# Optimization experiments

Hardware: AMD Instinct MI355X
Metric: run time of the kernel (lower is better)

## Reference

```python
import jax, jax.numpy as jnp
import numpy as np

N_QUBITS = 16
N_LAYERS = 2
NUM_CLASSES = 10
BATCH = 256

# CNOT as (c_out, t_out, c_in, t_in)
_CNOT = np.zeros((2, 2, 2, 2), dtype=np.complex64)
_CNOT[0, 0, 0, 0] = 1; _CNOT[0, 1, 0, 1] = 1
_CNOT[1, 1, 1, 0] = 1; _CNOT[1, 0, 1, 1] = 1
CNOT = jnp.asarray(_CNOT)


def rot_matrix(phi, theta, omega):
    # PennyLane Rot = RZ(omega) @ RY(theta) @ RZ(phi)
    c, s = jnp.cos(theta / 2), jnp.sin(theta / 2)
    m00 = jnp.exp(-0.5j * (phi + omega)) * c
    m01 = -jnp.exp(0.5j * (phi - omega)) * s
    m10 = jnp.exp(-0.5j * (phi - omega)) * s
    m11 = jnp.exp(0.5j * (phi + omega)) * c
    return jnp.stack([jnp.stack([m00, m01]), jnp.stack([m10, m11])]).astype(jnp.complex64)


def apply_1q(state, U, w, n):
    # state: (B, 2**n); wire 0 = most-significant bit (PennyLane convention)
    B = state.shape[0]
    st = state.reshape(B, 2 ** w, 2, -1)
    st = jnp.einsum('oi,baic->baoc', U, st)
    return st.reshape(B, -1)


def apply_cnot(state, c, t, n):
    B = state.shape[0]
    st = state.reshape((B,) + (2,) * n)
    st = jnp.tensordot(CNOT, st, axes=[[2, 3], [c + 1, t + 1]])  # new c,t axes at front
    st = jnp.moveaxis(st, [0, 1], [c + 1, t + 1])
    return st.reshape(B, -1)


def circuit_expvals(x, q_params, n, n_layers):
    # AmplitudeEmbedding with normalize=True
    norm = jnp.sqrt(jnp.sum(x * x, axis=-1, keepdims=True))
    psi = (x / norm).astype(jnp.complex64)
    for l in range(n_layers):
        for w in range(n):
            U = rot_matrix(q_params[l, w, 0], q_params[l, w, 1], q_params[l, w, 2])
            psi = apply_1q(psi, U, w, n)
        r = (l % (n - 1)) + 1  # default StronglyEntanglingLayers ranges
        for w in range(n):
            psi = apply_cnot(psi, w, (w + r) % n, n)
    probs = psi.real ** 2 + psi.imag ** 2  # (B, 2**n)
    B = probs.shape[0]
    ev = []
    for w in range(n):
        p = probs.reshape(B, 2 ** w, 2, -1)
        ev.append(p[:, :, 0, :].sum(axis=(1, 2)) - p[:, :, 1, :].sum(axis=(1, 2)))
    return jnp.stack(ev, axis=1)  # (B, n)


def setup_inputs() -> dict:
    key = jax.random.key(0)
    k1, k2, k3, k4 = jax.random.split(key, 4)
    x = jax.random.normal(k1, (BATCH, 2 ** N_QUBITS), dtype=jnp.float32)
    q_params = jax.random.normal(k2, (N_LAYERS, N_QUBITS, 3), dtype=jnp.float32)
    lim = 1.0 / np.sqrt(N_QUBITS)
    W = jax.random.uniform(k3, (NUM_CLASSES, N_QUBITS), jnp.float32, -lim, lim)
    b = jax.random.uniform(k4, (NUM_CLASSES,), jnp.float32, -lim, lim)
    return {"x": x, "q_params": q_params, "W": W, "b": b}


def reference(x, q_params, W, b):
    feats = circuit_expvals(x, q_params, N_QUBITS, N_LAYERS)  # (B, n_qubits)
    return feats @ W.T + b
```

## Files before the change

kernel.cpp:

```cpp
#include <hip/hip_runtime.h>


#define BATCH 256
#define NCLS 10

typedef float v2f __attribute__((ext_vector_type(2)));
typedef _Float16 f16x2 __attribute__((ext_vector_type(2)));

struct CircuitMeta { unsigned l1mask[16]; unsigned l1role[16]; unsigned fin[16]; };

__host__ __device__ constexpr CircuitMeta make_meta() {
  CircuitMeta m{};
  unsigned col[16], inv[16];
  for (int w = 0; w < 16; ++w) { col[w] = 1u << (15 - w); inv[w] = 1u << (15 - w); }
  for (int w = 0; w < 16; ++w) { int c = w, t = (w + 1) & 15; col[c] ^= col[t]; inv[t] ^= inv[c]; }
  for (int w = 0; w < 16; ++w) { m.l1mask[w] = col[w]; m.l1role[w] = inv[w]; }
  for (int w = 0; w < 16; ++w) { int c = w, t = (w + 2) & 15; col[c] ^= col[t]; inv[t] ^= inv[c]; }
  for (int w = 0; w < 16; ++w) m.fin[w] = inv[w];
  return m;
}
constexpr CircuitMeta META = make_meta();

__host__ __device__ constexpr unsigned HASH(unsigned i) {
  return i ^ ((i >> 4) & 15u) ^ ((i >> 8) & 15u);
}

__device__ __forceinline__ v2f swp(v2f a) { return __builtin_shufflevector(a, a, 1, 0); }

__device__ __forceinline__ unsigned PK(v2f a) {
  return __builtin_bit_cast(unsigned, __builtin_amdgcn_cvt_pkrtz(a.x, a.y));
}
__device__ __forceinline__ v2f UNPK(unsigned u) {
  f16x2 h = __builtin_bit_cast(f16x2, u);
  return (v2f){(float)h.x, (float)h.y};
}

template<int B0,int B1,int B2,int B3,int B4>
__host__ __device__ constexpr unsigned regval5(int j) {
  return ((unsigned)(j & 1) << B0) | ((unsigned)((j >> 1) & 1) << B1) |
         ((unsigned)((j >> 2) & 1) << B2) | ((unsigned)((j >> 3) & 1) << B3) |
         ((unsigned)((j >> 4) & 1) << B4);
}

template<int B0,int B1,int B2,int B3,int B4, unsigned MG, unsigned RG>
__device__ __forceinline__ void gate5(v2f (&A)[32], const float* __restrict__ g,
                                      int gi, unsigned tp) {
  constexpr unsigned cover = (1u<<B0)|(1u<<B1)|(1u<<B2)|(1u<<B3)|(1u<<B4);
  static_assert((MG & ~cover) == 0u, "gate mask not covered by stage reg bits");
  constexpr unsigned mr = ((MG>>B0)&1u) | (((MG>>B1)&1u)<<1) | (((MG>>B2)&1u)<<2)
                        | (((MG>>B3)&1u)<<3) | (((MG>>B4)&1u)<<4);
  static_assert(mr != 0u, "empty reg mask");
  constexpr unsigned pivot = mr & (0u - mr);

  float u00r = g[gi*8+0], u00i = g[gi*8+1], u01r = g[gi*8+2], u01i = g[gi*8+3];
  float u10r = g[gi*8+4], u10i = g[gi*8+5], u11r = g[gi*8+6], u11i = g[gi*8+7];
  const bool s = (__popc(RG & tp) & 1) != 0;
  float e00r = s ? u11r : u00r, e00i = s ? u11i : u00i;
  float e01r = s ? u10r : u01r, e01i = s ? u10i : u01i;
  float e10r = s ? u01r : u10r, e10i = s ? u01i : u10i;
  float e11r = s ? u00r : u11r, e11i = s ? u00i : u11i;
  v2f a00 = {e00r, e00r}, b00 = {-e00i, e00i};
  v2f a01 = {e01r, e01r}, b01 = {-e01i, e01i};
  v2f a10 = {e10r, e10r}, b10 = {-e10i, e10i};
  v2f a11 = {e11r, e11r}, b11 = {-e11i, e11i};

  #pragma unroll
  for (int j0 = 0; j0 < 32; ++j0) {
    if (j0 & (int)pivot) continue;
    const int j1 = j0 ^ (int)mr;
    const bool podd =
      (__builtin_popcount(RG & regval5<B0,B1,B2,B3,B4>(j0)) & 1) != 0;
    v2f v0 = A[j0], v1 = A[j1];
    v2f v0s = swp(v0), v1s = swp(v1);
    if (!podd) {
      A[j0] = a00*v0 + b00*v0s + a01*v1 + b01*v1s;
      A[j1] = a10*v0 + b10*v0s + a11*v1 + b11*v1s;
    } else {
      A[j0] = a11*v0 + b11*v0s + a10*v1 + b10*v1s;
      A[j1] = a01*v0 + b01*v0s + a00*v1 + b00*v1s;
    }
  }
}

__global__ void prep_gates(const float* __restrict__ qp, float* __restrict__ g) {
  int i = threadIdx.x;
  if (i >= 32) return;
  float phi = qp[i*3+0], th = qp[i*3+1], om = qp[i*3+2];
  float cth = cosf(0.5f*th), sth = sinf(0.5f*th);
  float a = 0.5f*(phi+om), d = 0.5f*(phi-om);
  float ca = cosf(a), sa = sinf(a), cd = cosf(d), sd = sinf(d);
  g[i*8+0] =  ca*cth; g[i*8+1] = -sa*cth;
  g[i*8+2] = -cd*sth; g[i*8+3] = -sd*sth;
  g[i*8+4] =  cd*sth; g[i*8+5] = -sd*sth;
  g[i*8+6] =  ca*cth; g[i*8+7] =  sa*cth;
}

__global__ __launch_bounds__(256, 4) void passA(const float* __restrict__ x,
    unsigned* __restrict__ st, const float* __restrict__ g) {
  __shared__ unsigned L[8192];
  const int t = threadIdx.x;
  const int batch = blockIdx.x >> 3;
  const unsigned f = blockIdx.x & 7;
  const float* xb = x + ((size_t)batch << 16) + ((size_t)f << 13);

  v2f A[32];
  #pragma unroll
  for (int j = 0; j < 32; ++j) A[j] = (v2f){xb[((unsigned)j << 8) | (unsigned)t], 0.f};

  gate5<8,9,10,11,12, 0x1000u,0x1000u>(A, g, 3, 0u);
  gate5<8,9,10,11,12, 0x0800u,0x0800u>(A, g, 4, 0u);
  gate5<8,9,10,11,12, 0x0400u,0x0400u>(A, g, 5, 0u);
  gate5<8,9,10,11,12, 0x0200u,0x0200u>(A, g, 6, 0u);
  gate5<8,9,10,11,12, 0x0100u,0x0100u>(A, g, 7, 0u);

  {
    const unsigned wb = HASH((unsigned)t);
    #pragma unroll
    for (int j = 0; j < 32; ++j) L[wb ^ HASH((unsigned)j << 8)] = PK(A[j]);
    __syncthreads();
    const unsigned rb = HASH((((unsigned)t & 0xF8u) << 5) | ((unsigned)t & 7u));
    #pragma unroll
    for (int j = 0; j < 32; ++j) A[j] = UNPK(L[rb ^ HASH((unsigned)j << 3)]);
  }

  gate5<3,4,5,6,7, 0x0080u,0x0080u>(A, g,  8, 0u);
  gate5<3,4,5,6,7, 0x0040u,0x0040u>(A, g,  9, 0u);
  gate5<3,4,5,6,7, 0x0020u,0x0020u>(A, g, 10, 0u);
  gate5<3,4,5,6,7, 0x0010u,0x0010u>(A, g, 11, 0u);
  gate5<3,4,5,6,7, 0x0008u,0x0008u>(A, g, 12, 0u);

  __syncthreads();
  {
    const unsigned wb = HASH((((unsigned)t & 0xF8u) << 5) | ((unsigned)t & 7u));
    #pragma unroll
    for (int j = 0; j < 32; ++j) L[wb ^ HASH((unsigned)j << 3)] = PK(A[j]);
    __syncthreads();
    const unsigned rb = HASH((unsigned)t << 3);
    #pragma unroll
    for (int j = 0; j < 32; ++j)
      A[j] = UNPK(L[rb ^ HASH(((unsigned)j & 7u) | (((unsigned)j & 24u) << 8))]);
  }

  gate5<0,1,2,11,12, 0x0004u,0x0004u>(A, g, 13, 0u);
  gate5<0,1,2,11,12, 0x0002u,0x0002u>(A, g, 14, 0u);
  gate5<0,1,2,11,12, 0x0001u,0x0001u>(A, g, 15, 0u);

  unsigned* outb = st + ((size_t)batch << 16) + ((size_t)f << 13);
  #pragma unroll
  for (int jh = 0; jh < 4; ++jh) {
    uint4 q0, q1;
    q0.x = PK(A[jh*8+0]); q0.y = PK(A[jh*8+1]); q0.z = PK(A[jh*8+2]); q0.w = PK(A[jh*8+3]);
    q1.x = PK(A[jh*8+4]); q1.y = PK(A[jh*8+5]); q1.z = PK(A[jh*8+6]); q1.w = PK(A[jh*8+7]);
    const unsigned si = ((unsigned)jh << 11) | ((unsigned)t << 3);
    *(uint4*)(outb + si) = q0;
    *(uint4*)(outb + si + 4) = q1;
  }
}

__global__ __launch_bounds__(256, 4) void passB(unsigned* __restrict__ st,
    const float* __restrict__ g) {
  __shared__ unsigned L[8192];
  const int t = threadIdx.x;
  const int batch = blockIdx.x >> 3;
  const unsigned c = blockIdx.x & 7;
  unsigned* stb = st + ((size_t)batch << 16);

  const unsigned lbase = ((unsigned)t & 127u) | (((unsigned)t & 128u) << 3) | (c << 7);
  v2f A[32];
  #pragma unroll
  for (int j = 0; j < 32; ++j) A[j] = UNPK(stb[((unsigned)j << 11) | lbase]);

  const unsigned tp1 = lbase;
  gate5<11,12,13,14,15, 0x8000u,0x8000u>(A, g, 0, tp1);
  gate5<11,12,13,14,15, 0x4000u,0x4000u>(A, g, 1, tp1);
  gate5<11,12,13,14,15, 0x2000u,0x2000u>(A, g, 2, tp1);
  gate5<11,12,13,14,15, META.l1mask[0], META.l1role[0]>(A, g, 16, tp1);
  gate5<11,12,13,14,15, META.l1mask[1], META.l1role[1]>(A, g, 17, tp1);
  gate5<11,12,13,14,15, META.l1mask[2], META.l1role[2]>(A, g, 18, tp1);
  gate5<11,12,13,14,15, META.l1mask[3], META.l1role[3]>(A, g, 19, tp1);

  {
    const unsigned wb = HASH((unsigned)t);
    #pragma unroll
    for (int j = 0; j < 32; ++j) L[wb ^ HASH((unsigned)j << 8)] = PK(A[j]);
    __syncthreads();
    const unsigned rb = HASH((((unsigned)t & 0xF0u) << 5) | (((unsigned)t & 15u) << 1));
    #pragma unroll
    for (int j = 0; j < 32; ++j)
      A[j] = UNPK(L[rb ^ HASH(((unsigned)j & 1u) | (((unsigned)j & 30u) << 4))]);
  }

  const unsigned tp2 = (((unsigned)t & 0xF0u) << 8) | (((unsigned)t & 15u) << 1) | (c << 7);
  gate5<0,5,6,10,11, META.l1mask[4], META.l1role[4]>(A, g, 20, tp2);
  gate5<0,5,6,10,11, META.l1mask[9], META.l1role[9]>(A, g, 25, tp2);

  __syncthreads();
  {
    const unsigned wb = HASH((((unsigned)t & 0xF0u) << 5) | (((unsigned)t & 15u) << 1));
    #pragma unroll
    for (int j = 0; j < 32; ++j)
      L[wb ^ HASH(((unsigned)j & 1u) | (((unsigned)j & 30u) << 4))] = PK(A[j]);
    __syncthreads();
    const unsigned rb = HASH((((unsigned)t & 0xFEu) << 5) | ((unsigned)t & 1u));
    #pragma unroll
    for (int j = 0; j < 32; ++j) A[j] = UNPK(L[rb ^ HASH((unsigned)j << 1)]);
  }

  const unsigned tp3 = (((unsigned)t & 0xFCu) << 8) | (((unsigned)t & 2u) << 5)
                     | ((unsigned)t & 1u) | (c << 7);
  gate5<1,2,3,4,5, META.l1mask[10], META.l1role[10]>(A, g, 26, tp3);
  gate5<1,2,3,4,5, META.l1mask[11], META.l1role[11]>(A, g, 27, tp3);
  gate5<1,2,3,4,5, META.l1mask[12], META.l1role[12]>(A, g, 28, tp3);
  gate5<1,2,3,4,5, META.l1mask[13], META.l1role[13]>(A, g, 29, tp3);

  __syncthreads();
  {
    const unsigned wb = HASH((((unsigned)t & 0xFEu) << 5) | ((unsigned)t & 1u));
    #pragma unroll
    for (int j = 0; j < 32; ++j) L[wb ^ HASH((unsigned)j << 1)] = PK(A[j]);
    __syncthreads();
    const unsigned rb = HASH((unsigned)t << 2);
    #pragma unroll
    for (int j = 0; j < 32; ++j)
      A[j] = UNPK(L[rb ^ HASH(((unsigned)j & 3u) | (((unsigned)j & 28u) << 8))]);
  }

  const unsigned tp4 = (((unsigned)t & 0xE0u) << 5) | (((unsigned)t & 31u) << 2) | (c << 7);
  gate5<0,1,13,14,15, META.l1mask[14], META.l1role[14]>(A, g, 30, tp4);
  gate5<0,1,13,14,15, META.l1mask[15], META.l1role[15]>(A, g, 31, tp4);

  #pragma unroll
  for (int jh = 0; jh < 8; ++jh) {
    uint4 q;
    q.x = PK(A[jh*4+0]); q.y = PK(A[jh*4+1]); q.z = PK(A[jh*4+2]); q.w = PK(A[jh*4+3]);
    *(uint4*)(stb + (tp4 | ((unsigned)jh << 13))) = q;
  }
}

__global__ __launch_bounds__(256, 4) void passC(const unsigned* __restrict__ st,
    const float* __restrict__ g, float* __restrict__ partials) {
  __shared__ float R[4][17];
  const int t = threadIdx.x;
  const int batch = blockIdx.x >> 3;
  const unsigned f = blockIdx.x & 7;
  const unsigned* stb = st + ((size_t)batch << 16);

  const unsigned cbase = (f << 13) | (((unsigned)t & 192u) << 5) | ((unsigned)t & 63u);
  v2f A[32];
  #pragma unroll
  for (int j = 0; j < 32; ++j) A[j] = UNPK(stb[cbase | ((unsigned)j << 6)]);

  gate5<6,7,8,9,10, META.l1mask[5], META.l1role[5]>(A, g, 21, cbase);
  gate5<6,7,8,9,10, META.l1mask[6], META.l1role[6]>(A, g, 22, cbase);
  gate5<6,7,8,9,10, META.l1mask[7], META.l1role[7]>(A, g, 23, cbase);
  gate5<6,7,8,9,10, META.l1mask[8], META.l1role[8]>(A, g, 24, cbase);

  float sv[16], tot = 0.f;
  #pragma unroll
  for (int w = 0; w < 16; ++w) sv[w] = 0.f;
  #pragma unroll
  for (int j = 0; j < 32; ++j) {
    const float pr = A[j].x*A[j].x + A[j].y*A[j].y;
    tot += pr;
    #pragma unroll
    for (int w = 0; w < 16; ++w) {
      const bool neg = (__builtin_popcount(META.fin[w] & ((unsigned)j << 6)) & 1) != 0;
      sv[w] += neg ? -pr : pr;
    }
  }
  #pragma unroll
  for (int w = 0; w < 16; ++w)
    if (__popc(META.fin[w] & cbase) & 1) sv[w] = -sv[w];

  #pragma unroll
  for (int off = 32; off; off >>= 1) {
    tot += __shfl_xor(tot, off, 64);
    #pragma unroll
    for (int w = 0; w < 16; ++w) sv[w] += __shfl_xor(sv[w], off, 64);
  }
  const int wave = t >> 6, lane = t & 63;
  if (lane == 0) {
    #pragma unroll
    for (int w = 0; w < 16; ++w) R[wave][w] = sv[w];
    R[wave][16] = tot;
  }
  __syncthreads();
  if (t < 17) {
    const float s2 = R[0][t] + R[1][t] + R[2][t] + R[3][t];
    partials[(size_t)blockIdx.x * 17 + t] = s2;
  }
}

__global__ __launch_bounds__(64) void head(const float* __restrict__ partials,
    const float* __restrict__ W, const float* __restrict__ bias,
    float* __restrict__ out) {
  const int b = blockIdx.x, tid = threadIdx.x;
  __shared__ float red[17];
  __shared__ float ev[16];
  if (tid < 17) {
    float s = 0.f;
    #pragma unroll
    for (int ch = 0; ch < 8; ++ch) s += partials[(size_t)((b << 3) + ch) * 17 + tid];
    red[tid] = s;
  }
  __syncthreads();
  if (tid < 16) ev[tid] = red[tid] / red[16];
  __syncthreads();
  if (tid < NCLS) {
    float o = bias[tid];
    #pragma unroll
    for (int w = 0; w < 16; ++w) o += ev[w] * W[tid*16 + w];
    out[b*NCLS + tid] = o;
  }
}

extern "C" void kernel_launch(void* const* d_in, const int* in_sizes, int n_in,
                              void* d_out, int out_size, void* d_ws, size_t ws_size,
                              hipStream_t stream) {
  const float* x  = (const float*)d_in[0];
  const float* qp = (const float*)d_in[1];
  const float* W  = (const float*)d_in[2];
  const float* bv = (const float*)d_in[3];
  float* out = (float*)d_out;

  unsigned* st     = (unsigned*)d_ws;
  float*    gates  = (float*)((char*)d_ws + (size_t)BATCH * 65536 * 4);
  float*    parts  = (float*)((char*)gates + 1024);

  prep_gates<<<dim3(1), dim3(64), 0, stream>>>(qp, gates);
  passA<<<dim3(BATCH*8), dim3(256), 0, stream>>>(x, st, gates);
  passB<<<dim3(BATCH*8), dim3(256), 0, stream>>>(st, gates);
  passC<<<dim3(BATCH*8), dim3(256), 0, stream>>>(st, gates, parts);
  head<<<dim3(BATCH), dim3(64), 0, stream>>>(parts, W, bv, out);
}
```

Before: 207.8 us.

## Switch state registers to split real/imag planes for packed FMA gates

The per-thread state moves from 32 interleaved complex values to 16 real and 16 imaginary two-wide vectors, where the two lanes hold a pair of amplitudes differing in one qubit bit. The gate kernel is rewritten for this layout, with separate paths for register-pair, lane-only and mixed gates, so the complex arithmetic maps onto packed FMA without swaps for most gates. All loads, LDS transposes and stores are rewritten to pack and unpack the new layout, and the final reduction is vectorised too. The goal is fewer VALU instructions per gate; the cost is more complex coefficient setup and possible register pressure.

```diff
diff --git a/kernel.cpp b/kernel.cpp
--- a/kernel.cpp
+++ b/kernel.cpp
@@ -6,6 +6,8 @@
 
 typedef float v2f __attribute__((ext_vector_type(2)));
 typedef _Float16 f16x2 __attribute__((ext_vector_type(2)));
+
+#define KATTR __launch_bounds__(256, 4)
 
 struct CircuitMeta { unsigned l1mask[16]; unsigned l1role[16]; unsigned fin[16]; };
 
@@ -25,61 +27,126 @@
   return i ^ ((i >> 4) & 15u) ^ ((i >> 8) & 15u);
 }
 
+__device__ __forceinline__ unsigned PKS(float r, float i) {
+  return __builtin_bit_cast(unsigned, __builtin_amdgcn_cvt_pkrtz(r, i));
+}
+__device__ __forceinline__ v2f vfma(v2f a, v2f b, v2f c) {
+  return __builtin_elementwise_fma(a, b, c);
+}
 __device__ __forceinline__ v2f swp(v2f a) { return __builtin_shufflevector(a, a, 1, 0); }
 
-__device__ __forceinline__ unsigned PK(v2f a) {
-  return __builtin_bit_cast(unsigned, __builtin_amdgcn_cvt_pkrtz(a.x, a.y));
-}
-__device__ __forceinline__ v2f UNPK(unsigned u) {
-  f16x2 h = __builtin_bit_cast(f16x2, u);
-  return (v2f){(float)h.x, (float)h.y};
-}
-
-template<int B0,int B1,int B2,int B3,int B4>
-__host__ __device__ constexpr unsigned regval5(int j) {
-  return ((unsigned)(j & 1) << B0) | ((unsigned)((j >> 1) & 1) << B1) |
-         ((unsigned)((j >> 2) & 1) << B2) | ((unsigned)((j >> 3) & 1) << B3) |
-         ((unsigned)((j >> 4) & 1) << B4);
-}
-
-template<int B0,int B1,int B2,int B3,int B4, unsigned MG, unsigned RG>
-__device__ __forceinline__ void gate5(v2f (&A)[32], const float* __restrict__ g,
+__device__ __forceinline__ float esel(int q, int pos, float e00, float e01,
+                                      float e10, float e11) {
+  int p = q ? 3 - pos : pos;
+  return p == 0 ? e00 : p == 1 ? e01 : p == 2 ? e10 : e11;
+}
+
+template<int KB0,int KB1,int KB2,int KB3,int LB, unsigned MG, unsigned RG>
+__device__ __forceinline__ void gateV(v2f (&Vr)[16], v2f (&Vi)[16],
+                                      const float* __restrict__ g,
                                       int gi, unsigned tp) {
-  constexpr unsigned cover = (1u<<B0)|(1u<<B1)|(1u<<B2)|(1u<<B3)|(1u<<B4);
+  constexpr unsigned cover = (1u<<KB0)|(1u<<KB1)|(1u<<KB2)|(1u<<KB3)|(1u<<LB);
   static_assert((MG & ~cover) == 0u, "gate mask not covered by stage reg bits");
-  constexpr unsigned mr = ((MG>>B0)&1u) | (((MG>>B1)&1u)<<1) | (((MG>>B2)&1u)<<2)
-                        | (((MG>>B3)&1u)<<3) | (((MG>>B4)&1u)<<4);
-  static_assert(mr != 0u, "empty reg mask");
-  constexpr unsigned pivot = mr & (0u - mr);
+  constexpr unsigned mk = ((MG>>KB0)&1u) | (((MG>>KB1)&1u)<<1)
+                        | (((MG>>KB2)&1u)<<2) | (((MG>>KB3)&1u)<<3);
+  constexpr int ml = (int)((MG>>LB)&1u);
+  constexpr unsigned rk = ((RG>>KB0)&1u) | (((RG>>KB1)&1u)<<1)
+                        | (((RG>>KB2)&1u)<<2) | (((RG>>KB3)&1u)<<3);
+  constexpr int rl = (int)((RG>>LB)&1u);
+  static_assert(mk != 0u || ml != 0, "empty mask");
 
   float u00r = g[gi*8+0], u00i = g[gi*8+1], u01r = g[gi*8+2], u01i = g[gi*8+3];
   float u10r = g[gi*8+4], u10i = g[gi*8+5], u11r = g[gi*8+6], u11i = g[gi*8+7];
   const bool s = (__popc(RG & tp) & 1) != 0;
-  float e00r = s ? u11r : u00r, e00i = s ? u11i : u00i;
-  float e01r = s ? u10r : u01r, e01i = s ? u10i : u01i;
-  float e10r = s ? u01r : u10r, e10i = s ? u01i : u10i;
-  float e11r = s ? u00r : u11r, e11i = s ? u00i : u11i;
-  v2f a00 = {e00r, e00r}, b00 = {-e00i, e00i};
-  v2f a01 = {e01r, e01r}, b01 = {-e01i, e01i};
-  v2f a10 = {e10r, e10r}, b10 = {-e10i, e10i};
-  v2f a11 = {e11r, e11r}, b11 = {-e11i, e11i};
-
-  #pragma unroll
-  for (int j0 = 0; j0 < 32; ++j0) {
-    if (j0 & (int)pivot) continue;
-    const int j1 = j0 ^ (int)mr;
-    const bool podd =
-      (__builtin_popcount(RG & regval5<B0,B1,B2,B3,B4>(j0)) & 1) != 0;
-    v2f v0 = A[j0], v1 = A[j1];
-    v2f v0s = swp(v0), v1s = swp(v1);
-    if (!podd) {
-      A[j0] = a00*v0 + b00*v0s + a01*v1 + b01*v1s;
-      A[j1] = a10*v0 + b10*v0s + a11*v1 + b11*v1s;
-    } else {
-      A[j0] = a11*v0 + b11*v0s + a10*v1 + b10*v1s;
-      A[j1] = a01*v0 + b01*v0s + a00*v1 + b00*v1s;
-    }
-  }
+  float e00r = s?u11r:u00r, e00i = s?u11i:u00i;
+  float e01r = s?u10r:u01r, e01i = s?u10i:u01i;
+  float e10r = s?u01r:u10r, e10i = s?u01i:u10i;
+  float e11r = s?u00r:u11r, e11i = s?u00i:u11i;
+  #define ER(q,pos) esel((q),(pos),e00r,e01r,e10r,e11r)
+  #define EI(q,pos) esel((q),(pos),e00i,e01i,e10i,e11i)
+
+  if constexpr (ml == 0) {
+    static_assert((__builtin_popcount(rk & mk) & 1) == 1, "pair parity invariant");
+    v2f c00r = {ER(0,0), ER(rl,0)}, c00i = {EI(0,0), EI(rl,0)};
+    v2f c01r = {ER(0,1), ER(rl,1)}, c01i = {EI(0,1), EI(rl,1)};
+    v2f c10r = {ER(0,2), ER(rl,2)}, c10i = {EI(0,2), EI(rl,2)};
+    v2f c11r = {ER(0,3), ER(rl,3)}, c11i = {EI(0,3), EI(rl,3)};
+    constexpr unsigned pivot = mk & (0u - mk);
+    #pragma unroll
+    for (int k0 = 0; k0 < 16; ++k0) {
+      if (k0 & (int)pivot) continue;
+      const int k1 = k0 ^ (int)mk;
+      const bool podd = (__builtin_popcount(rk & (unsigned)k0) & 1) != 0;
+      const v2f A0r = podd?c11r:c00r, A0i = podd?c11i:c00i;
+      const v2f A1r = podd?c10r:c01r, A1i = podd?c10i:c01i;
+      const v2f B0r = podd?c01r:c10r, B0i = podd?c01i:c10i;
+      const v2f B1r = podd?c00r:c11r, B1i = podd?c00i:c11i;
+      const v2f v0r = Vr[k0], v0i = Vi[k0], v1r = Vr[k1], v1i = Vi[k1];
+      v2f n0r = A0r*v0r; n0r = vfma(-A0i, v0i, n0r);
+      n0r = vfma(A1r, v1r, n0r); n0r = vfma(-A1i, v1i, n0r);
+      v2f n0i = A0r*v0i; n0i = vfma(A0i, v0r, n0i);
+      n0i = vfma(A1r, v1i, n0i); n0i = vfma(A1i, v1r, n0i);
+      v2f n1r = B0r*v0r; n1r = vfma(-B0i, v0i, n1r);
+      n1r = vfma(B1r, v1r, n1r); n1r = vfma(-B1i, v1i, n1r);
+      v2f n1i = B0r*v0i; n1i = vfma(B0i, v0r, n1i);
+      n1i = vfma(B1r, v1i, n1i); n1i = vfma(B1i, v1r, n1i);
+      Vr[k0] = n0r; Vi[k0] = n0i; Vr[k1] = n1r; Vi[k1] = n1i;
+    }
+  } else if constexpr (mk == 0u) {
+    static_assert(rl == 1, "lane-only gate requires rl==1");
+    v2f CA0r = {ER(0,0), ER(1,0)}, CA0i = {EI(0,0), EI(1,0)};
+    v2f CB0r = {ER(0,1), ER(1,1)}, CB0i = {EI(0,1), EI(1,1)};
+    v2f CA1r = {ER(1,0), ER(0,0)}, CA1i = {EI(1,0), EI(0,0)};
+    v2f CB1r = {ER(1,1), ER(0,1)}, CB1i = {EI(1,1), EI(0,1)};
+    #pragma unroll
+    for (int k = 0; k < 16; ++k) {
+      const bool q = (__builtin_popcount(rk & (unsigned)k) & 1) != 0;
+      const v2f CAr = q?CA1r:CA0r, CAi = q?CA1i:CA0i;
+      const v2f CBr = q?CB1r:CB0r, CBi = q?CB1i:CB0i;
+      const v2f vr = Vr[k], vi = Vi[k];
+      const v2f svr = swp(vr), svi = swp(vi);
+      v2f nr = CAr*vr; nr = vfma(-CAi, vi, nr);
+      nr = vfma(CBr, svr, nr); nr = vfma(-CBi, svi, nr);
+      v2f ni = CAr*vi; ni = vfma(CAi, vr, ni);
+      ni = vfma(CBr, svi, ni); ni = vfma(CBi, svr, ni);
+      Vr[k] = nr; Vi[k] = ni;
+    }
+  } else {
+    constexpr int dm = __builtin_popcount(rk & mk) & 1;
+    static_assert((dm ^ rl) == 1, "cross gate pair parity invariant");
+    v2f CA0r = {ER(0,0), ER(rl,0)},          CA0i = {EI(0,0), EI(rl,0)};
+    v2f CB0r = {ER(0,1), ER(rl,1)},          CB0i = {EI(0,1), EI(rl,1)};
+    v2f CC0r = {ER(dm,0), ER(dm^rl,0)},      CC0i = {EI(dm,0), EI(dm^rl,0)};
+    v2f CD0r = {ER(dm,1), ER(dm^rl,1)},      CD0i = {EI(dm,1), EI(dm^rl,1)};
+    v2f CA1r = {ER(1,0), ER(1^rl,0)},        CA1i = {EI(1,0), EI(1^rl,0)};
+    v2f CB1r = {ER(1,1), ER(1^rl,1)},        CB1i = {EI(1,1), EI(1^rl,1)};
+    v2f CC1r = {ER(1^dm,0), ER(1^dm^rl,0)},  CC1i = {EI(1^dm,0), EI(1^dm^rl,0)};
+    v2f CD1r = {ER(1^dm,1), ER(1^dm^rl,1)},  CD1i = {EI(1^dm,1), EI(1^dm^rl,1)};
+    constexpr unsigned pivot = mk & (0u - mk);
+    #pragma unroll
+    for (int k0 = 0; k0 < 16; ++k0) {
+      if (k0 & (int)pivot) continue;
+      const int k1 = k0 ^ (int)mk;
+      const bool q = (__builtin_popcount(rk & (unsigned)k0) & 1) != 0;
+      const v2f CAr = q?CA1r:CA0r, CAi = q?CA1i:CA0i;
+      const v2f CBr = q?CB1r:CB0r, CBi = q?CB1i:CB0i;
+      const v2f CCr = q?CC1r:CC0r, CCi = q?CC1i:CC0i;
+      const v2f CDr = q?CD1r:CD0r, CDi = q?CD1i:CD0i;
+      const v2f vr = Vr[k0], vi = Vi[k0], ur = Vr[k1], ui = Vi[k1];
+      const v2f sur = swp(ur), sui = swp(ui), svr = swp(vr), svi = swp(vi);
+      v2f nvr = CAr*vr; nvr = vfma(-CAi, vi, nvr);
+      nvr = vfma(CBr, sur, nvr); nvr = vfma(-CBi, sui, nvr);
+      v2f nvi = CAr*vi; nvi = vfma(CAi, vr, nvi);
+      nvi = vfma(CBr, sui, nvi); nvi = vfma(CBi, sur, nvi);
+      v2f nur = CCr*ur; nur = vfma(-CCi, ui, nur);
+      nur = vfma(CDr, svr, nur); nur = vfma(-CDi, svi, nur);
+      v2f nui = CCr*ui; nui = vfma(CCi, ur, nui);
+      nui = vfma(CDr, svi, nui); nui = vfma(CDi, svr, nui);
+      Vr[k0] = nvr; Vi[k0] = nvi; Vr[k1] = nur; Vi[k1] = nui;
+    }
+  }
+  #undef ER
+  #undef EI
 }
 
 __global__ void prep_gates(const float* __restrict__ qp, float* __restrict__ g) {
@@ -95,7 +162,11 @@
   g[i*8+6] =  ca*cth; g[i*8+7] =  sa*cth;
 }
 
-__global__ __launch_bounds__(256, 4) void passA(const float* __restrict__ x,
+__device__ __forceinline__ unsigned PKL(v2f r, v2f i, int l) {
+  return l ? PKS(r.y, i.y) : PKS(r.x, i.x);
+}
+
+__global__ KATTR void passA(const float* __restrict__ x,
     unsigned* __restrict__ st, const float* __restrict__ g) {
   __shared__ unsigned L[8192];
   const int t = threadIdx.x;
@@ -103,61 +174,86 @@
   const unsigned f = blockIdx.x & 7;
   const float* xb = x + ((size_t)batch << 16) + ((size_t)f << 13);
 
-  v2f A[32];
-  #pragma unroll
-  for (int j = 0; j < 32; ++j) A[j] = (v2f){xb[((unsigned)j << 8) | (unsigned)t], 0.f};
-
-  gate5<8,9,10,11,12, 0x1000u,0x1000u>(A, g, 3, 0u);
-  gate5<8,9,10,11,12, 0x0800u,0x0800u>(A, g, 4, 0u);
-  gate5<8,9,10,11,12, 0x0400u,0x0400u>(A, g, 5, 0u);
-  gate5<8,9,10,11,12, 0x0200u,0x0200u>(A, g, 6, 0u);
-  gate5<8,9,10,11,12, 0x0100u,0x0100u>(A, g, 7, 0u);
+  v2f Vr[16], Vi[16];
+  #pragma unroll
+  for (int k = 0; k < 16; ++k) {
+    Vr[k] = (v2f){xb[((unsigned)k << 9) | (unsigned)t],
+                  xb[((unsigned)k << 9) | 256u | (unsigned)t]};
+    Vi[k] = (v2f){0.f, 0.f};
+  }
+
+  gateV<9,10,11,12,8, 0x1000u,0x1000u>(Vr, Vi, g, 3, 0u);
+  gateV<9,10,11,12,8, 0x0800u,0x0800u>(Vr, Vi, g, 4, 0u);
+  gateV<9,10,11,12,8, 0x0400u,0x0400u>(Vr, Vi, g, 5, 0u);
+  gateV<9,10,11,12,8, 0x0200u,0x0200u>(Vr, Vi, g, 6, 0u);
+  gateV<9,10,11,12,8, 0x0100u,0x0100u>(Vr, Vi, g, 7, 0u);
 
   {
     const unsigned wb = HASH((unsigned)t);
     #pragma unroll
-    for (int j = 0; j < 32; ++j) L[wb ^ HASH((unsigned)j << 8)] = PK(A[j]);
+    for (int k = 0; k < 16; ++k) {
+      L[wb ^ HASH(((unsigned)k << 9))]        = PKL(Vr[k], Vi[k], 0);
+      L[wb ^ HASH(((unsigned)k << 9) | 256u)] = PKL(Vr[k], Vi[k], 1);
+    }
     __syncthreads();
     const unsigned rb = HASH((((unsigned)t & 0xF8u) << 5) | ((unsigned)t & 7u));
     #pragma unroll
-    for (int j = 0; j < 32; ++j) A[j] = UNPK(L[rb ^ HASH((unsigned)j << 3)]);
-  }
-
-  gate5<3,4,5,6,7, 0x0080u,0x0080u>(A, g,  8, 0u);
-  gate5<3,4,5,6,7, 0x0040u,0x0040u>(A, g,  9, 0u);
-  gate5<3,4,5,6,7, 0x0020u,0x0020u>(A, g, 10, 0u);
-  gate5<3,4,5,6,7, 0x0010u,0x0010u>(A, g, 11, 0u);
-  gate5<3,4,5,6,7, 0x0008u,0x0008u>(A, g, 12, 0u);
+    for (int k = 0; k < 16; ++k) {
+      f16x2 h0 = __builtin_bit_cast(f16x2, L[rb ^ HASH(((unsigned)k << 4))]);
+      f16x2 h1 = __builtin_bit_cast(f16x2, L[rb ^ HASH(((unsigned)k << 4) | 8u)]);
+      Vr[k] = (v2f){(float)h0.x, (float)h1.x};
+      Vi[k] = (v2f){(float)h0.y, (float)h1.y};
+    }
+  }
+
+  gateV<4,5,6,7,3, 0x0080u,0x0080u>(Vr, Vi, g,  8, 0u);
+  gateV<4,5,6,7,3, 0x0040u,0x0040u>(Vr, Vi, g,  9, 0u);
+  gateV<4,5,6,7,3, 0x0020u,0x0020u>(Vr, Vi, g, 10, 0u);
+  gateV<4,5,6,7,3, 0x0010u,0x0010u>(Vr, Vi, g, 11, 0u);
+  gateV<4,5,6,7,3, 0x0008u,0x0008u>(Vr, Vi, g, 12, 0u);
 
   __syncthreads();
   {
     const unsigned wb = HASH((((unsigned)t & 0xF8u) << 5) | ((unsigned)t & 7u));
     #pragma unroll
-    for (int j = 0; j < 32; ++j) L[wb ^ HASH((unsigned)j << 3)] = PK(A[j]);
+    for (int k = 0; k < 16; ++k) {
+      L[wb ^ HASH(((unsigned)k << 4))]      = PKL(Vr[k], Vi[k], 0);
+      L[wb ^ HASH(((unsigned)k << 4) | 8u)] = PKL(Vr[k], Vi[k], 1);
+    }
     __syncthreads();
     const unsigned rb = HASH((unsigned)t << 3);
     #pragma unroll
-    for (int j = 0; j < 32; ++j)
-      A[j] = UNPK(L[rb ^ HASH(((unsigned)j & 7u) | (((unsigned)j & 24u) << 8))]);
-  }
-
-  gate5<0,1,2,11,12, 0x0004u,0x0004u>(A, g, 13, 0u);
-  gate5<0,1,2,11,12, 0x0002u,0x0002u>(A, g, 14, 0u);
-  gate5<0,1,2,11,12, 0x0001u,0x0001u>(A, g, 15, 0u);
+    for (int k = 0; k < 16; ++k) {
+      const unsigned kv = ((unsigned)k & 7u) | (((unsigned)k & 8u) << 8);
+      f16x2 h0 = __builtin_bit_cast(f16x2, L[rb ^ HASH(kv)]);
+      f16x2 h1 = __builtin_bit_cast(f16x2, L[rb ^ HASH(kv | 4096u)]);
+      Vr[k] = (v2f){(float)h0.x, (float)h1.x};
+      Vi[k] = (v2f){(float)h0.y, (float)h1.y};
+    }
+  }
+
+  gateV<0,1,2,11,12, 0x0004u,0x0004u>(Vr, Vi, g, 13, 0u);
+  gateV<0,1,2,11,12, 0x0002u,0x0002u>(Vr, Vi, g, 14, 0u);
+  gateV<0,1,2,11,12, 0x0001u,0x0001u>(Vr, Vi, g, 15, 0u);
 
   unsigned* outb = st + ((size_t)batch << 16) + ((size_t)f << 13);
   #pragma unroll
-  for (int jh = 0; jh < 4; ++jh) {
-    uint4 q0, q1;
-    q0.x = PK(A[jh*8+0]); q0.y = PK(A[jh*8+1]); q0.z = PK(A[jh*8+2]); q0.w = PK(A[jh*8+3]);
-    q1.x = PK(A[jh*8+4]); q1.y = PK(A[jh*8+5]); q1.z = PK(A[jh*8+6]); q1.w = PK(A[jh*8+7]);
-    const unsigned si = ((unsigned)jh << 11) | ((unsigned)t << 3);
-    *(uint4*)(outb + si) = q0;
-    *(uint4*)(outb + si + 4) = q1;
-  }
-}
-
-__global__ __launch_bounds__(256, 4) void passB(unsigned* __restrict__ st,
+  for (int l = 0; l < 2; ++l) {
+    #pragma unroll
+    for (int kh = 0; kh < 2; ++kh) {
+      uint4 q0, q1;
+      q0.x = PKL(Vr[kh*8+0], Vi[kh*8+0], l); q0.y = PKL(Vr[kh*8+1], Vi[kh*8+1], l);
+      q0.z = PKL(Vr[kh*8+2], Vi[kh*8+2], l); q0.w = PKL(Vr[kh*8+3], Vi[kh*8+3], l);
+      q1.x = PKL(Vr[kh*8+4], Vi[kh*8+4], l); q1.y = PKL(Vr[kh*8+5], Vi[kh*8+5], l);
+      q1.z = PKL(Vr[kh*8+6], Vi[kh*8+6], l); q1.w = PKL(Vr[kh*8+7], Vi[kh*8+7], l);
+      const unsigned si = ((unsigned)l << 12) | ((unsigned)kh << 11) | ((unsigned)t << 3);
+      *(uint4*)(outb + si) = q0;
+      *(uint4*)(outb + si + 4) = q1;
+    }
+  }
+}
+
+__global__ KATTR void passB(unsigned* __restrict__ st,
     const float* __restrict__ g) {
   __shared__ unsigned L[8192];
   const int t = threadIdx.x;
@@ -166,78 +262,109 @@
   unsigned* stb = st + ((size_t)batch << 16);
 
   const unsigned lbase = ((unsigned)t & 127u) | (((unsigned)t & 128u) << 3) | (c << 7);
-  v2f A[32];
-  #pragma unroll
-  for (int j = 0; j < 32; ++j) A[j] = UNPK(stb[((unsigned)j << 11) | lbase]);
+  v2f Vr[16], Vi[16];
+  #pragma unroll
+  for (int k = 0; k < 16; ++k) {
+    f16x2 h0 = __builtin_bit_cast(f16x2, stb[((unsigned)k << 12) | lbase]);
+    f16x2 h1 = __builtin_bit_cast(f16x2, stb[((unsigned)k << 12) | 2048u | lbase]);
+    Vr[k] = (v2f){(float)h0.x, (float)h1.x};
+    Vi[k] = (v2f){(float)h0.y, (float)h1.y};
+  }
 
   const unsigned tp1 = lbase;
-  gate5<11,12,13,14,15, 0x8000u,0x8000u>(A, g, 0, tp1);
-  gate5<11,12,13,14,15, 0x4000u,0x4000u>(A, g, 1, tp1);
-  gate5<11,12,13,14,15, 0x2000u,0x2000u>(A, g, 2, tp1);
-  gate5<11,12,13,14,15, META.l1mask[0], META.l1role[0]>(A, g, 16, tp1);
-  gate5<11,12,13,14,15, META.l1mask[1], META.l1role[1]>(A, g, 17, tp1);
-  gate5<11,12,13,14,15, META.l1mask[2], META.l1role[2]>(A, g, 18, tp1);
-  gate5<11,12,13,14,15, META.l1mask[3], META.l1role[3]>(A, g, 19, tp1);
+  gateV<12,13,14,15,11, 0x8000u,0x8000u>(Vr, Vi, g, 0, tp1);
+  gateV<12,13,14,15,11, 0x4000u,0x4000u>(Vr, Vi, g, 1, tp1);
+  gateV<12,13,14,15,11, 0x2000u,0x2000u>(Vr, Vi, g, 2, tp1);
+  gateV<12,13,14,15,11, META.l1mask[0], META.l1role[0]>(Vr, Vi, g, 16, tp1);
+  gateV<12,13,14,15,11, META.l1mask[1], META.l1role[1]>(Vr, Vi, g, 17, tp1);
+  gateV<12,13,14,15,11, META.l1mask[2], META.l1role[2]>(Vr, Vi, g, 18, tp1);
+  gateV<12,13,14,15,11, META.l1mask[3], META.l1role[3]>(Vr, Vi, g, 19, tp1);
 
   {
     const unsigned wb = HASH((unsigned)t);
     #pragma unroll
-    for (int j = 0; j < 32; ++j) L[wb ^ HASH((unsigned)j << 8)] = PK(A[j]);
+    for (int k = 0; k < 16; ++k) {
+      L[wb ^ HASH(((unsigned)k << 9))]        = PKL(Vr[k], Vi[k], 0);
+      L[wb ^ HASH(((unsigned)k << 9) | 256u)] = PKL(Vr[k], Vi[k], 1);
+    }
     __syncthreads();
     const unsigned rb = HASH((((unsigned)t & 0xF0u) << 5) | (((unsigned)t & 15u) << 1));
     #pragma unroll
-    for (int j = 0; j < 32; ++j)
-      A[j] = UNPK(L[rb ^ HASH(((unsigned)j & 1u) | (((unsigned)j & 30u) << 4))]);
+    for (int k = 0; k < 16; ++k) {
+      f16x2 h0 = __builtin_bit_cast(f16x2, L[rb ^ HASH(((unsigned)k << 5))]);
+      f16x2 h1 = __builtin_bit_cast(f16x2, L[rb ^ HASH(((unsigned)k << 5) | 1u)]);
+      Vr[k] = (v2f){(float)h0.x, (float)h1.x};
+      Vi[k] = (v2f){(float)h0.y, (float)h1.y};
+    }
   }
 
   const unsigned tp2 = (((unsigned)t & 0xF0u) << 8) | (((unsigned)t & 15u) << 1) | (c << 7);
-  gate5<0,5,6,10,11, META.l1mask[4], META.l1role[4]>(A, g, 20, tp2);
-  gate5<0,5,6,10,11, META.l1mask[9], META.l1role[9]>(A, g, 25, tp2);
+  gateV<5,6,10,11,0, META.l1mask[4], META.l1role[4]>(Vr, Vi, g, 20, tp2);
+  gateV<5,6,10,11,0, META.l1mask[9], META.l1role[9]>(Vr, Vi, g, 25, tp2);
 
   __syncthreads();
   {
     const unsigned wb = HASH((((unsigned)t & 0xF0u) << 5) | (((unsigned)t & 15u) << 1));
     #pragma unroll
-    for (int j = 0; j < 32; ++j)
-      L[wb ^ HASH(((unsigned)j & 1u) | (((unsigned)j & 30u) << 4))] = PK(A[j]);
+    for (int k = 0; k < 16; ++k) {
+      L[wb ^ HASH(((unsigned)k << 5))]      = PKL(Vr[k], Vi[k], 0);
+      L[wb ^ HASH(((unsigned)k << 5) | 1u)] = PKL(Vr[k], Vi[k], 1);
+    }
     __syncthreads();
     const unsigned rb = HASH((((unsigned)t & 0xFEu) << 5) | ((unsigned)t & 1u));
     #pragma unroll
-    for (int j = 0; j < 32; ++j) A[j] = UNPK(L[rb ^ HASH((unsigned)j << 1)]);
+    for (int k = 0; k < 16; ++k) {
+      f16x2 h0 = __builtin_bit_cast(f16x2, L[rb ^ HASH(((unsigned)k << 2))]);
+      f16x2 h1 = __builtin_bit_cast(f16x2, L[rb ^ HASH(((unsigned)k << 2) | 2u)]);
+      Vr[k] = (v2f){(float)h0.x, (float)h1.x};
+      Vi[k] = (v2f){(float)h0.y, (float)h1.y};
+    }
   }
 
   const unsigned tp3 = (((unsigned)t & 0xFCu) << 8) | (((unsigned)t & 2u) << 5)
                      | ((unsigned)t & 1u) | (c << 7);
-  gate5<1,2,3,4,5, META.l1mask[10], META.l1role[10]>(A, g, 26, tp3);
-  gate5<1,2,3,4,5, META.l1mask[11], META.l1role[11]>(A, g, 27, tp3);
-  gate5<1,2,3,4,5, META.l1mask[12], META.l1role[12]>(A, g, 28, tp3);
-  gate5<1,2,3,4,5, META.l1mask[13], META.l1role[13]>(A, g, 29, tp3);
+  gateV<2,3,4,5,1, META.l1mask[10], META.l1role[10]>(Vr, Vi, g, 26, tp3);
+  gateV<2,3,4,5,1, META.l1mask[11], META.l1role[11]>(Vr, Vi, g, 27, tp3);
+  gateV<2,3,4,5,1, META.l1mask[12], META.l1role[12]>(Vr, Vi, g, 28, tp3);
+  gateV<2,3,4,5,1, META.l1mask[13], META.l1role[13]>(Vr, Vi, g, 29, tp3);
 
   __syncthreads();
   {
     const unsigned wb = HASH((((unsigned)t & 0xFEu) << 5) | ((unsigned)t & 1u));
     #pragma unroll
-    for (int j = 0; j < 32; ++j) L[wb ^ HASH((unsigned)j << 1)] = PK(A[j]);
+    for (int k = 0; k < 16; ++k) {
+      L[wb ^ HASH(((unsigned)k << 2))]      = PKL(Vr[k], Vi[k], 0);
+      L[wb ^ HASH(((unsigned)k << 2) | 2u)] = PKL(Vr[k], Vi[k], 1);
+    }
     __syncthreads();
     const unsigned rb = HASH((unsigned)t << 2);
     #pragma unroll
-    for (int j = 0; j < 32; ++j)
-      A[j] = UNPK(L[rb ^ HASH(((unsigned)j & 3u) | (((unsigned)j & 28u) << 8))]);
+    for (int k = 0; k < 16; ++k) {
+      const unsigned kv = ((unsigned)k & 3u) | (((unsigned)k & 12u) << 9);
+      f16x2 h0 = __builtin_bit_cast(f16x2, L[rb ^ HASH(kv)]);
+      f16x2 h1 = __builtin_bit_cast(f16x2, L[rb ^ HASH(kv | 1024u)]);
+      Vr[k] = (v2f){(float)h0.x, (float)h1.x};
+      Vi[k] = (v2f){(float)h0.y, (float)h1.y};
+    }
   }
 
   const unsigned tp4 = (((unsigned)t & 0xE0u) << 5) | (((unsigned)t & 31u) << 2) | (c << 7);
-  gate5<0,1,13,14,15, META.l1mask[14], META.l1role[14]>(A, g, 30, tp4);
-  gate5<0,1,13,14,15, META.l1mask[15], META.l1role[15]>(A, g, 31, tp4);
-
-  #pragma unroll
-  for (int jh = 0; jh < 8; ++jh) {
-    uint4 q;
-    q.x = PK(A[jh*4+0]); q.y = PK(A[jh*4+1]); q.z = PK(A[jh*4+2]); q.w = PK(A[jh*4+3]);
-    *(uint4*)(stb + (tp4 | ((unsigned)jh << 13))) = q;
-  }
-}
-
-__global__ __launch_bounds__(256, 4) void passC(const unsigned* __restrict__ st,
+  gateV<0,1,14,15,13, META.l1mask[14], META.l1role[14]>(Vr, Vi, g, 30, tp4);
+  gateV<0,1,14,15,13, META.l1mask[15], META.l1role[15]>(Vr, Vi, g, 31, tp4);
+
+  #pragma unroll
+  for (int l = 0; l < 2; ++l) {
+    #pragma unroll
+    for (int kh = 0; kh < 4; ++kh) {
+      uint4 q;
+      q.x = PKL(Vr[kh*4+0], Vi[kh*4+0], l); q.y = PKL(Vr[kh*4+1], Vi[kh*4+1], l);
+      q.z = PKL(Vr[kh*4+2], Vi[kh*4+2], l); q.w = PKL(Vr[kh*4+3], Vi[kh*4+3], l);
+      *(uint4*)(stb + (tp4 | ((unsigned)l << 13) | ((unsigned)kh << 14))) = q;
+    }
+  }
+}
+
+__global__ KATTR void passC(const unsigned* __restrict__ st,
     const float* __restrict__ g, float* __restrict__ partials) {
   __shared__ float R[4][17];
   const int t = threadIdx.x;
@@ -246,28 +373,42 @@
   const unsigned* stb = st + ((size_t)batch << 16);
 
   const unsigned cbase = (f << 13) | (((unsigned)t & 192u) << 5) | ((unsigned)t & 63u);
-  v2f A[32];
-  #pragma unroll
-  for (int j = 0; j < 32; ++j) A[j] = UNPK(stb[cbase | ((unsigned)j << 6)]);
-
-  gate5<6,7,8,9,10, META.l1mask[5], META.l1role[5]>(A, g, 21, cbase);
-  gate5<6,7,8,9,10, META.l1mask[6], META.l1role[6]>(A, g, 22, cbase);
-  gate5<6,7,8,9,10, META.l1mask[7], META.l1role[7]>(A, g, 23, cbase);
-  gate5<6,7,8,9,10, META.l1mask[8], META.l1role[8]>(A, g, 24, cbase);
-
-  float sv[16], tot = 0.f;
-  #pragma unroll
-  for (int w = 0; w < 16; ++w) sv[w] = 0.f;
-  #pragma unroll
-  for (int j = 0; j < 32; ++j) {
-    const float pr = A[j].x*A[j].x + A[j].y*A[j].y;
-    tot += pr;
+  v2f Vr[16], Vi[16];
+  #pragma unroll
+  for (int k = 0; k < 16; ++k) {
+    f16x2 h0 = __builtin_bit_cast(f16x2, stb[cbase | ((unsigned)k << 7)]);
+    f16x2 h1 = __builtin_bit_cast(f16x2, stb[cbase | ((unsigned)k << 7) | 64u]);
+    Vr[k] = (v2f){(float)h0.x, (float)h1.x};
+    Vi[k] = (v2f){(float)h0.y, (float)h1.y};
+  }
+
+  gateV<7,8,9,10,6, META.l1mask[5], META.l1role[5]>(Vr, Vi, g, 21, cbase);
+  gateV<7,8,9,10,6, META.l1mask[6], META.l1role[6]>(Vr, Vi, g, 22, cbase);
+  gateV<7,8,9,10,6, META.l1mask[7], META.l1role[7]>(Vr, Vi, g, 23, cbase);
+  gateV<7,8,9,10,6, META.l1mask[8], META.l1role[8]>(Vr, Vi, g, 24, cbase);
+
+  v2f sv2[16], tot2 = (v2f){0.f, 0.f};
+  #pragma unroll
+  for (int w = 0; w < 16; ++w) sv2[w] = (v2f){0.f, 0.f};
+  const v2f lm = (v2f){1.f, -1.f};
+  #pragma unroll
+  for (int k = 0; k < 16; ++k) {
+    v2f pr = vfma(Vi[k], Vi[k], Vr[k]*Vr[k]);
+    tot2 = tot2 + pr;
+    v2f prm = pr * lm;
     #pragma unroll
     for (int w = 0; w < 16; ++w) {
-      const bool neg = (__builtin_popcount(META.fin[w] & ((unsigned)j << 6)) & 1) != 0;
-      sv[w] += neg ? -pr : pr;
-    }
-  }
+      const unsigned m = META.fin[w];
+      const bool fl = ((m >> 6) & 1u) != 0;
+      const bool sk = (__builtin_popcount(m & ((unsigned)k << 7)) & 1) != 0;
+      const v2f term = fl ? prm : pr;
+      sv2[w] = sk ? (sv2[w] - term) : (sv2[w] + term);
+    }
+  }
+  float sv[16];
+  #pragma unroll
+  for (int w = 0; w < 16; ++w) sv[w] = sv2[w].x + sv2[w].y;
+  float tot = tot2.x + tot2.y;
   #pragma unroll
   for (int w = 0; w < 16; ++w)
     if (__popc(META.fin[w] & cbase) & 1) sv[w] = -sv[w];
```

New measurement: 203.7 us. 1.02x faster.
